# Kernel optimization log

Measured on AMD Instinct MI355X. Metric: run time of the kernel, lower is better.

Reference implementation:

```python
import jax, jax.numpy as jnp
import numpy as np

EMBED_DIM = 256
NUM_HEADS = 8
HEAD_DIM = EMBED_DIM // NUM_HEADS
SCALE = HEAD_DIM ** -0.5  # note: scale uses head_dim even though attention is over full D
EPS = 1e-12  # torch F.normalize eps


def setup_inputs() -> dict:
    key = jax.random.key(0)
    k1, k2, k3 = jax.random.split(key, 3)
    B, Nq, Nk, D = 4, 4096, 4096, EMBED_DIM
    return {
        "query": jax.random.normal(k1, (B, Nq, D), dtype=jnp.float32),
        "key": jax.random.normal(k2, (B, Nk, D), dtype=jnp.float32),
        "value": jax.random.normal(k3, (B, Nk, D), dtype=jnp.float32),
    }


def _l2_normalize(x):
    # matches torch.nn.functional.normalize(x, dim=-1): x / max(||x||, eps)
    n = jnp.linalg.norm(x, axis=-1, keepdims=True)
    return x / jnp.maximum(n, EPS)


def reference(query, key, value):
    q = _l2_normalize(query)          # (B, Nq, D)
    k = _l2_normalize(key)            # (B, Nk, D)
    scores = jnp.einsum("bqd,bkd->bqk", q, k) * SCALE  # (B, Nq, Nk) cosine sims
    attn = jax.nn.softmax(scores, axis=-1)
    return jnp.einsum("bqk,bkd->bqd", attn, value)     # (B, Nq, D)
```

## Files before the change

### kernel.cpp

```cpp
#include <hip/hip_runtime.h>


#define NQ 4096
#define DIM 256
#define NROWS 16384
#define BM 64
#define BN 64
#define KSPLIT 2
#define NITER 32
#define PSTRIDE 68

typedef __attribute__((ext_vector_type(8))) short bf16x8;
typedef __attribute__((ext_vector_type(4))) float f32x4;
typedef __attribute__((ext_vector_type(16))) float f32x16;

__device__ __forceinline__ unsigned short f2bf(float f) {
  unsigned int u = __float_as_uint(f);
  u += 0x7fffu + ((u >> 16) & 1u);
  return (unsigned short)(u >> 16);
}

__device__ __forceinline__ float bf2f(unsigned short h) {
  return __uint_as_float((unsigned int)h << 16);
}

__device__ __forceinline__ unsigned int pack2bf(float a, float b) {
  unsigned int ua = __float_as_uint(a) + 0x8000u;
  unsigned int ub = __float_as_uint(b) + 0x8000u;
  return __builtin_amdgcn_perm(ub, ua, 0x07060302u);
}

__device__ __forceinline__ void gload16(const void* g, void* l) {
  __builtin_amdgcn_global_load_lds(
      (const __attribute__((address_space(1))) unsigned int*)g,
      (__attribute__((address_space(3))) unsigned int*)l, 16, 0, 0);
}

__global__ __launch_bounds__(256) void prep(
    const float* __restrict__ K, const float* __restrict__ V,
    unsigned short* __restrict__ Kfm, unsigned short* __restrict__ Vfm)
{
  __shared__ unsigned short vt[32 * 264];
  const int blk = blockIdx.x, tid = threadIdx.x;
  const int wave = tid >> 6, lane = tid & 63;
  if (blk < 512) {
    const int kt2 = blk;
    const int kt = kt2 >> 1, h = kt2 & 1;
    #pragma unroll
    for (int i = 0; i < 8; i++) {
      const int r = wave*8 + i;
      float4 v = *(const float4*)(K + ((size_t)kt2*32 + r) * DIM + lane * 4);
      float ss = v.x*v.x + v.y*v.y + v.z*v.z + v.w*v.w;
      #pragma unroll
      for (int off = 1; off < 64; off <<= 1) ss += __shfl_xor(ss, off, 64);
      float scale = 1.0f / fmaxf(sqrtf(ss), 1e-12f);
      ushort4 o;
      o.x = f2bf(v.x*scale); o.y = f2bf(v.y*scale);
      o.z = f2bf(v.z*scale); o.w = f2bf(v.w*scale);
      *(ushort4*)(vt + r*264 + lane*4) = o;
    }
    __syncthreads();
    #pragma unroll
    for (int s = 0; s < 4; s++) {
      const int ch = tid + 256*s;
      const int c = ch >> 5, r = ch & 31;
      const int n = h*32 + r;
      bf16x8 val = *(const bf16x8*)(vt + r*264 + c*8);
      *(bf16x8*)(Kfm + (size_t)kt*16384 + (size_t)(c*64 + n)*8) = val;
    }
  } else {
    const int NS = blk - 512;
    #pragma unroll
    for (int i = 0; i < 4; i++) {
      const int e = tid + 256*i;
      const int nl = e >> 6, d = (e & 63) * 4;
      float4 v = *(const float4*)(V + ((size_t)NS*16 + nl)*DIM + d);
      ushort4 o;
      o.x = f2bf(v.x); o.y = f2bf(v.y); o.z = f2bf(v.z); o.w = f2bf(v.w);
      *(ushort4*)(vt + nl*264 + d) = o;
    }
    __syncthreads();
    #pragma unroll
    for (int i = 0; i < 2; i++) {
      const int ch = tid + 256*i;
      const int db = ch >> 6, ln = ch & 63;
      const int row0 = (ln >> 5) * 8, dd = db*32 + (ln & 31);
      ushort4 a, b;
      a.x = vt[(row0+0)*264 + dd]; a.y = vt[(row0+1)*264 + dd];
      a.z = vt[(row0+2)*264 + dd]; a.w = vt[(row0+3)*264 + dd];
      b.x = vt[(row0+4)*264 + dd]; b.y = vt[(row0+5)*264 + dd];
      b.z = vt[(row0+6)*264 + dd]; b.w = vt[(row0+7)*264 + dd];
      size_t base = ((size_t)(NS*8 + db)*64 + ln)*8;
      *(ushort4*)(Vfm + base)     = a;
      *(ushort4*)(Vfm + base + 4) = b;
    }
  }
}

__global__ __launch_bounds__(256, 2) void attn(
    const float* __restrict__ Qg,
    const unsigned short* __restrict__ Kfm,
    const unsigned short* __restrict__ Vfm,
    unsigned short* __restrict__ Opart, float* __restrict__ lpart)
{
  __shared__ unsigned short Klds[2][32 * 64 * 8];
  __shared__ unsigned short Plds[BM * PSTRIDE];

  const int tid = threadIdx.x, wave = tid >> 6, lane = tid & 63;
  const int l15 = lane & 15, l4 = lane >> 4;
  const int blk = blockIdx.x;
  const int g = blk & 7, qt = blk >> 3;
  const int b = g >> 1, ks = g & 1;
  const int Rq0 = b*NQ + qt*BM;
  const int n0base = b*NQ + ks*(NQ/KSPLIT);
  const int mi = wave & 1, ni = wave >> 1;

  {
    unsigned short* Qlds = &Klds[0][0];
    #pragma unroll
    for (int i = 0; i < 16; i++) {
      const int r = wave*16 + i;
      float4 v = *(const float4*)(Qg + (size_t)(Rq0 + r)*DIM + lane*4);
      float ss = v.x*v.x + v.y*v.y + v.z*v.z + v.w*v.w;
      #pragma unroll
      for (int off = 1; off < 64; off <<= 1) ss += __shfl_xor(ss, off, 64);
      float scale = (0.17677669529663687f * 1.4426950408889634f)
                    / fmaxf(sqrtf(ss), 1e-12f);
      ushort4 o;
      o.x = f2bf(v.x*scale); o.y = f2bf(v.y*scale);
      o.z = f2bf(v.z*scale); o.w = f2bf(v.w*scale);
      *(ushort4*)(Qlds + r*DIM + lane*4) = o;
    }
  }
  __syncthreads();

  bf16x8 qf[2][8];
  #pragma unroll
  for (int mt = 0; mt < 2; mt++) {
    const unsigned short* qrow = &Klds[0][0] + (mi*32 + mt*16 + l15)*DIM + l4*8;
    #pragma unroll
    for (int kg = 0; kg < 8; kg++)
      qf[mt][kg] = *(const bf16x8*)(qrow + kg*32);
  }
  __syncthreads();

  f32x16 oacc[2][2] = {};
  float lacc[2] = {};

  auto stage = [&](int kt_) {
    unsigned short* dst = &Klds[kt_ & 1][0];
    const unsigned short* src = Kfm + (size_t)((n0base + kt_*BN) >> 6) * (32*64*8);
    #pragma unroll
    for (int jj = 0; jj < 4; jj++) {
      const int c = wave*8 + jj*2;
      gload16(src + (size_t)c*512 + lane*8,     dst + (size_t)c*512);
      gload16(src + (size_t)(c+1)*512 + lane*8, dst + (size_t)(c+1)*512);
    }
  };

  stage(0);

  for (int kt = 0; kt < NITER; kt++) {
    __syncthreads();

    if (kt + 1 < NITER) stage(kt + 1);
    __builtin_amdgcn_sched_barrier(0);

    const unsigned short* kb = &Klds[kt & 1][0];

    f32x4 sacc[2][2] = {};
    #pragma unroll
    for (int kg = 0; kg < 8; kg++) {
      bf16x8 kf[2];
      #pragma unroll
      for (int nt = 0; nt < 2; nt++) {
        const int nrow = ni*32 + nt*16 + l15;
        const int c = kg*4 + l4;
        kf[nt] = *(const bf16x8*)(kb + ((size_t)(c*64 + nrow))*8);
      }
      __builtin_amdgcn_s_setprio(1);
      #pragma unroll
      for (int nt = 0; nt < 2; nt++)
        #pragma unroll
        for (int mt = 0; mt < 2; mt++)
          sacc[nt][mt] = __builtin_amdgcn_mfma_f32_16x16x32_bf16(
              kf[nt], qf[mt][kg], sacc[nt][mt], 0, 0, 0);
      __builtin_amdgcn_s_setprio(0);
    }

    #pragma unroll
    for (int nt = 0; nt < 2; nt++)
      #pragma unroll
      for (int mt = 0; mt < 2; mt++) {
        float p0 = __builtin_amdgcn_exp2f(sacc[nt][mt][0]);
        float p1 = __builtin_amdgcn_exp2f(sacc[nt][mt][1]);
        float p2 = __builtin_amdgcn_exp2f(sacc[nt][mt][2]);
        float p3 = __builtin_amdgcn_exp2f(sacc[nt][mt][3]);
        lacc[mt] += (p0 + p1) + (p2 + p3);
        uint2 pk;
        pk.x = pack2bf(p0, p1);
        pk.y = pack2bf(p2, p3);
        const int m = mi*32 + mt*16 + l15;
        const int n = ni*32 + nt*16 + 4*l4;
        *(uint2*)(Plds + m*PSTRIDE + n) = pk;
      }

    asm volatile("s_waitcnt lgkmcnt(0)" ::: "memory");
    __builtin_amdgcn_s_barrier();
    __builtin_amdgcn_sched_barrier(0);

    const int NB0 = (n0base + kt*BN) >> 4;
    bf16x8 pf[2][2], vf[2][2];
    #pragma unroll
    for (int mt2 = 0; mt2 < 2; mt2++)
      pf[0][mt2] = *(const bf16x8*)(Plds + (mt2*32 + (lane & 31))*PSTRIDE
                                    + 8*(lane >> 5));
    #pragma unroll
    for (int dt = 0; dt < 2; dt++)
      vf[0][dt] = *(const bf16x8*)(Vfm + ((size_t)(NB0*8 + wave*2 + dt)*64 + lane)*8);
    #pragma unroll
    for (int kstep = 0; kstep < 4; kstep++) {
      const int cb = kstep & 1;
      if (kstep < 3) {
        #pragma unroll
        for (int mt2 = 0; mt2 < 2; mt2++)
          pf[cb^1][mt2] = *(const bf16x8*)(Plds + (mt2*32 + (lane & 31))*PSTRIDE
                                           + (kstep+1)*16 + 8*(lane >> 5));
        #pragma unroll
        for (int dt = 0; dt < 2; dt++)
          vf[cb^1][dt] = *(const bf16x8*)(Vfm
              + ((size_t)((NB0 + kstep + 1)*8 + wave*2 + dt)*64 + lane)*8);
      }
      __builtin_amdgcn_s_setprio(1);
      #pragma unroll
      for (int mt2 = 0; mt2 < 2; mt2++)
        #pragma unroll
        for (int dt = 0; dt < 2; dt++)
          oacc[mt2][dt] = __builtin_amdgcn_mfma_f32_32x32x16_bf16(
              pf[cb][mt2], vf[cb][dt], oacc[mt2][dt], 0, 0, 0);
      __builtin_amdgcn_s_setprio(0);
    }
  }

  #pragma unroll
  for (int mt = 0; mt < 2; mt++) {
    float s = lacc[mt];
    s += __shfl_xor(s, 16, 64);
    s += __shfl_xor(s, 32, 64);
    if (l4 == 0)
      lpart[(size_t)(ks*2 + ni)*NROWS + Rq0 + mi*32 + mt*16 + l15] = s;
  }

  #pragma unroll
  for (int mt2 = 0; mt2 < 2; mt2++)
    #pragma unroll
    for (int dt = 0; dt < 2; dt++)
      #pragma unroll
      for (int reg = 0; reg < 16; reg++) {
        const int m = mt2*32 + 4*(lane >> 5) + (reg & 3) + 8*(reg >> 2);
        const int d = wave*64 + dt*32 + (lane & 31);
        Opart[((size_t)(ks*NROWS + Rq0 + m))*DIM + d] = f2bf(oacc[mt2][dt][reg]);
      }
}

__global__ __launch_bounds__(256) void combine(
    const unsigned short* __restrict__ Opart, const float* __restrict__ lpart,
    float* __restrict__ out)
{
  const size_t idx = (size_t)blockIdx.x*256 + threadIdx.x;
  const size_t e = idx*4;
  const int R = (int)(e >> 8);
  ushort4 o0 = *(const ushort4*)(Opart + e);
  ushort4 o1 = *(const ushort4*)(Opart + (size_t)NROWS*DIM + e);
  float ls = lpart[R] + lpart[NROWS + R] + lpart[2*NROWS + R] + lpart[3*NROWS + R];
  float inv = 1.0f / ls;
  float4 o;
  o.x = (bf2f(o0.x) + bf2f(o1.x))*inv;
  o.y = (bf2f(o0.y) + bf2f(o1.y))*inv;
  o.z = (bf2f(o0.z) + bf2f(o1.z))*inv;
  o.w = (bf2f(o0.w) + bf2f(o1.w))*inv;
  *(float4*)(out + e) = o;
}

extern "C" void kernel_launch(void* const* d_in, const int* in_sizes, int n_in,
                              void* d_out, int out_size, void* d_ws, size_t ws_size,
                              hipStream_t stream) {
  const float* Q = (const float*)d_in[0];
  const float* K = (const float*)d_in[1];
  const float* V = (const float*)d_in[2];
  char* ws = (char*)d_ws;
  unsigned short* Kfm   = (unsigned short*)(ws);
  unsigned short* Vfm   = (unsigned short*)(ws + 8388608);
  unsigned short* Opart = (unsigned short*)(ws + 16777216);
  float* lpart = (float*)(ws + 33554432);

  prep<<<1536, 256, 0, stream>>>(K, V, Kfm, Vfm);
  attn<<<512, 256, 0, stream>>>(Q, Kfm, Vfm, Opart, lpart);
  combine<<<4096, 256, 0, stream>>>(Opart, lpart, (float*)d_out);
}
```

Before: 173.9 us.

## Hoist V loads ahead of QK and stagger K-tile order across query blocks

Each iteration now issues all V-fragment global loads at its start, so they overlap the QK MFMA and softmax instead of being fetched inside the PV loop. The K-staging barrier becomes an explicit vmcnt wait plus s_barrier, and all P fragments are loaded from LDS before the PV MFMAs run. Query-tile groups start at different K tiles (phase offset, wrapping modulo NITER), which spreads concurrent blocks over different K/V memory regions. This raises register pressure from holding 8 V and 8 P fragments, and its correctness depends on the vmcnt(16) count matching the number of outstanding loads. The final iteration also issues a redundant stage of the wrapped-around tile.

Measured after the change: 173.8 us. Within noise of the previous version (-0.1%).

```diff
diff --git a/kernel.cpp b/kernel.cpp
--- a/kernel.cpp
+++ b/kernel.cpp
@@ -114,6 +114,7 @@
   const int Rq0 = b*NQ + qt*BM;
   const int n0base = b*NQ + ks*(NQ/KSPLIT);
   const int mi = wave & 1, ni = wave >> 1;
+  const int phase = ((qt >> 5) & 1) * (NITER/2);
 
   {
     unsigned short* Qlds = &Klds[0][0];
@@ -147,9 +148,10 @@
   f32x16 oacc[2][2] = {};
   float lacc[2] = {};
 
-  auto stage = [&](int kt_) {
-    unsigned short* dst = &Klds[kt_ & 1][0];
-    const unsigned short* src = Kfm + (size_t)((n0base + kt_*BN) >> 6) * (32*64*8);
+  auto stage = [&](int it_) {
+    const int tile = (it_ + phase) & (NITER - 1);
+    unsigned short* dst = &Klds[it_ & 1][0];
+    const unsigned short* src = Kfm + (size_t)((n0base >> 6) + tile) * (32*64*8);
     #pragma unroll
     for (int jj = 0; jj < 4; jj++) {
       const int c = wave*8 + jj*2;
@@ -160,13 +162,26 @@
 
   stage(0);
 
-  for (int kt = 0; kt < NITER; kt++) {
-    __syncthreads();
-
-    if (kt + 1 < NITER) stage(kt + 1);
+  for (int it = 0; it < NITER; it++) {
+    const int kt = (it + phase) & (NITER - 1);
+
+    const int NB0 = (n0base + kt*BN) >> 4;
+    bf16x8 vf[4][2];
+    #pragma unroll
+    for (int kstep = 0; kstep < 4; kstep++)
+      #pragma unroll
+      for (int dt = 0; dt < 2; dt++)
+        vf[kstep][dt] = *(const bf16x8*)(Vfm
+            + ((size_t)((NB0 + kstep)*8 + wave*2 + dt)*64 + lane)*8);
+
+    stage((it + 1) & (NITER - 1));
     __builtin_amdgcn_sched_barrier(0);
 
-    const unsigned short* kb = &Klds[kt & 1][0];
+    asm volatile("s_waitcnt vmcnt(16)" ::: "memory");
+    __builtin_amdgcn_s_barrier();
+    __builtin_amdgcn_sched_barrier(0);
+
+    const unsigned short* kb = &Klds[it & 1][0];
 
     f32x4 sacc[2][2] = {};
     #pragma unroll
@@ -209,35 +224,22 @@
     __builtin_amdgcn_s_barrier();
     __builtin_amdgcn_sched_barrier(0);
 
-    const int NB0 = (n0base + kt*BN) >> 4;
-    bf16x8 pf[2][2], vf[2][2];
-    #pragma unroll
-    for (int mt2 = 0; mt2 < 2; mt2++)
-      pf[0][mt2] = *(const bf16x8*)(Plds + (mt2*32 + (lane & 31))*PSTRIDE
-                                    + 8*(lane >> 5));
-    #pragma unroll
-    for (int dt = 0; dt < 2; dt++)
-      vf[0][dt] = *(const bf16x8*)(Vfm + ((size_t)(NB0*8 + wave*2 + dt)*64 + lane)*8);
+    bf16x8 pf[4][2];
+    #pragma unroll
+    for (int kstep = 0; kstep < 4; kstep++)
+      #pragma unroll
+      for (int mt2 = 0; mt2 < 2; mt2++)
+        pf[kstep][mt2] = *(const bf16x8*)(Plds + (mt2*32 + (lane & 31))*PSTRIDE
+                                          + kstep*16 + 8*(lane >> 5));
     #pragma unroll
     for (int kstep = 0; kstep < 4; kstep++) {
-      const int cb = kstep & 1;
-      if (kstep < 3) {
-        #pragma unroll
-        for (int mt2 = 0; mt2 < 2; mt2++)
-          pf[cb^1][mt2] = *(const bf16x8*)(Plds + (mt2*32 + (lane & 31))*PSTRIDE
-                                           + (kstep+1)*16 + 8*(lane >> 5));
-        #pragma unroll
-        for (int dt = 0; dt < 2; dt++)
-          vf[cb^1][dt] = *(const bf16x8*)(Vfm
-              + ((size_t)((NB0 + kstep + 1)*8 + wave*2 + dt)*64 + lane)*8);
-      }
       __builtin_amdgcn_s_setprio(1);
       #pragma unroll
       for (int mt2 = 0; mt2 < 2; mt2++)
         #pragma unroll
         for (int dt = 0; dt < 2; dt++)
           oacc[mt2][dt] = __builtin_amdgcn_mfma_f32_32x32x16_bf16(
-              pf[cb][mt2], vf[cb][dt], oacc[mt2][dt], 0, 0, 0);
+              pf[kstep][mt2], vf[kstep][dt], oacc[mt2][dt], 0, 0, 0);
       __builtin_amdgcn_s_setprio(0);
     }
   }
```
